# Performance work log

Measured on AMD Instinct MI355X. Metric: run time of the kernel, lower is better.

Reference implementation:

```python
import jax, jax.numpy as jnp
import numpy as np

N_NODES = 50000
N_EDGES = 800000
IN_CH = 512
HID = 256


def setup_inputs() -> dict:
    key = jax.random.key(0)
    ks = jax.random.split(key, 8)
    x = jax.random.normal(ks[0], (N_NODES, IN_CH), dtype=jnp.float32)
    edge_index = jax.random.randint(ks[1], (2, N_EDGES), 0, N_NODES, dtype=jnp.int64)
    # Glorot-ish init for weights
    W0 = jax.random.normal(ks[2], (IN_CH, HID), dtype=jnp.float32) / np.sqrt(IN_CH)
    W1 = jax.random.normal(ks[3], (HID, HID), dtype=jnp.float32) / np.sqrt(HID)
    W2 = jax.random.normal(ks[4], (HID, HID), dtype=jnp.float32) / np.sqrt(HID)
    Wout = jax.random.normal(ks[5], (HID, 1), dtype=jnp.float32) / np.sqrt(HID)
    return {
        "x": x, "edge_index": edge_index,
        "W0": W0, "b0": jnp.zeros((HID,), jnp.float32),
        "W1": W1, "b1": jnp.zeros((HID,), jnp.float32),
        "W2": W2, "b2": jnp.zeros((HID,), jnp.float32),
        "Wout": Wout, "bout": jnp.zeros((1,), jnp.float32),
    }


def _gcn_norm(edge_index, num_nodes):
    # Add self-loops, compute symmetric normalization D^-1/2 (A+I) D^-1/2
    loops = jnp.arange(num_nodes, dtype=edge_index.dtype)
    src = jnp.concatenate([edge_index[0], loops])
    dst = jnp.concatenate([edge_index[1], loops])
    ones = jnp.ones(src.shape[0], dtype=jnp.float32)
    deg = jax.ops.segment_sum(ones, dst, num_segments=num_nodes)
    dinv = jnp.where(deg > 0, jax.lax.rsqrt(deg), 0.0)
    norm = dinv[src] * dinv[dst]  # [E + N]
    return src, dst, norm


def _gcn_conv(x, src, dst, norm, W, b, num_nodes):
    h = x @ W                              # [N, out] dense GEMM first (PyG order)
    msg = h[src] * norm[:, None]           # gather + scale
    agg = jax.ops.segment_sum(msg, dst, num_segments=num_nodes)  # scatter-add
    return agg + b


def reference(x, edge_index, W0, b0, W1, b1, W2, b2, Wout, bout):
    n = x.shape[0]
    src, dst, norm = _gcn_norm(edge_index, n)
    h = jax.nn.relu(_gcn_conv(x, src, dst, norm, W0, b0, n))
    h = jax.nn.relu(_gcn_conv(h, src, dst, norm, W1, b1, n))
    h = jax.nn.relu(_gcn_conv(h, src, dst, norm, W2, b2, n))
    out = h @ Wout + bout                  # [N, 1] readout
    return out[:, 0]                       # squeeze(-1) -> [N]
```

## Files before the change

kernel.cpp:

```cpp
#include <hip/hip_runtime.h>

#define HID 256
#define IN_CH 512
#define NPAD 50176

typedef __attribute__((ext_vector_type(8))) short s16x8;
typedef __attribute__((ext_vector_type(4))) float f32x4;
typedef __attribute__((ext_vector_type(4))) _Float16 f16x4;

#define GLBP(p) ((const __attribute__((address_space(1))) void*)(p))
#define LDSP(p) ((__attribute__((address_space(3))) void*)(p))


__global__ __launch_bounds__(256) void k_count(const int* __restrict__ dst,
                                               int* __restrict__ cnt, int E) {
    int e = blockIdx.x * 256 + threadIdx.x;
    if (e < E) atomicAdd(&cnt[dst[e]], 1);
}

__global__ __launch_bounds__(256) void k_scan_bsum(const int* __restrict__ cnt,
                                                   int* __restrict__ bsum, int n) {
    __shared__ int sdata[256];
    int t = threadIdx.x;
    int base = blockIdx.x * 1024 + t * 4;
    int s = 0;
#pragma unroll
    for (int j = 0; j < 4; ++j) if (base + j < n) s += cnt[base + j];
    sdata[t] = s;
    __syncthreads();
    for (int off = 128; off > 0; off >>= 1) {
        if (t < off) sdata[t] += sdata[t + off];
        __syncthreads();
    }
    if (t == 0) bsum[blockIdx.x] = sdata[0];
}

__global__ __launch_bounds__(64) void k_scan_boff(const int* __restrict__ bsum,
                                                  int* __restrict__ boff, int nb) {
    int lane = threadIdx.x;
    int own = (lane < nb) ? bsum[lane] : 0;
    int v = own;
    for (int off = 1; off < 64; off <<= 1) {
        int u = __shfl_up(v, off, 64);
        if (lane >= off) v += u;
    }
    if (lane < nb) boff[lane] = v - own;
}

__global__ __launch_bounds__(256) void k_scan_write(const int* __restrict__ cnt,
                                                    const int* __restrict__ boff,
                                                    int* __restrict__ rowptr,
                                                    float* __restrict__ dinv, int n) {
    __shared__ int sdata[256];
    int t = threadIdx.x;
    int base = blockIdx.x * 1024 + t * 4;
    int c0 = (base + 0 < n) ? cnt[base + 0] : 0;
    int c1 = (base + 1 < n) ? cnt[base + 1] : 0;
    int c2 = (base + 2 < n) ? cnt[base + 2] : 0;
    int c3 = (base + 3 < n) ? cnt[base + 3] : 0;
    int tsum = c0 + c1 + c2 + c3;
    sdata[t] = tsum;
    __syncthreads();
    for (int off = 1; off < 256; off <<= 1) {
        int v = (t >= off) ? sdata[t - off] : 0;
        __syncthreads();
        if (t >= off) sdata[t] += v;
        __syncthreads();
    }
    int excl = sdata[t] - tsum;
    int p = boff[blockIdx.x] + excl;
    if (base + 0 < n) { rowptr[base + 1] = p + c0;                dinv[base + 0] = rsqrtf((float)(c0 + 1)); }
    if (base + 1 < n) { rowptr[base + 2] = p + c0 + c1;           dinv[base + 1] = rsqrtf((float)(c1 + 1)); }
    if (base + 2 < n) { rowptr[base + 3] = p + c0 + c1 + c2;      dinv[base + 2] = rsqrtf((float)(c2 + 1)); }
    if (base + 3 < n) { rowptr[base + 4] = p + c0 + c1 + c2 + c3; dinv[base + 3] = rsqrtf((float)(c3 + 1)); }
    if (blockIdx.x == 0 && t == 0) rowptr[0] = 0;
}

__global__ __launch_bounds__(256) void k_fill(const int* __restrict__ src,
                                              const int* __restrict__ dst,
                                              const int* __restrict__ rowptr,
                                              int* __restrict__ cursor,
                                              const float* __restrict__ dinv,
                                              int2* __restrict__ erec, int E) {
    int e = blockIdx.x * 256 + threadIdx.x;
    if (e >= E) return;
    int d = dst[e];
    int s = src[e];
    int pos = rowptr[d] + atomicAdd(&cursor[d], 1);
    float w = dinv[s] * dinv[d];
    erec[pos] = make_int2(s, __float_as_int(w));
}


__device__ __forceinline__ void wsplit_one(const float* W, unsigned short* Bt, int idx) {
    int n = idx & 255;
    int k = idx >> 8;
    float w = W[(size_t)k * HID + n];
    unsigned int u = __float_as_uint(w);
    unsigned short hi = (unsigned short)(u >> 16);
    float hif = __uint_as_float(u & 0xffff0000u);
    float lo = w - hif;
    unsigned short lob = (unsigned short)(__float_as_uint(lo) >> 16);
    unsigned short* p = Bt + (size_t)(k >> 5) * (HID * 104) + n * 104 + 3 * (k & 31);
    p[0] = hi; p[1] = hi; p[2] = lob;
}

__global__ __launch_bounds__(256) void k_wsplit3(const float* __restrict__ W0,
                                                 const float* __restrict__ W1,
                                                 const float* __restrict__ W2,
                                                 unsigned short* __restrict__ Bt0,
                                                 unsigned short* __restrict__ Bt1,
                                                 unsigned short* __restrict__ Bt2) {
    int t = blockIdx.x * 256 + threadIdx.x;
    if (t < IN_CH * HID) wsplit_one(W0, Bt0, t);
    else if (t < IN_CH * HID + HID * HID) wsplit_one(W1, Bt1, t - IN_CH * HID);
    else wsplit_one(W2, Bt2, t - IN_CH * HID - HID * HID);
}


template<bool RELU>
__global__ __launch_bounds__(512, 6) void k_gemm_mfma(const float* __restrict__ A,
                                                      const unsigned short* __restrict__ Bt,
                                                      _Float16* __restrict__ C16,
                                                      int M, int Korig) {
    __shared__ unsigned short Als[128 * 104];
    __shared__ unsigned short Bls[128 * 104];

    const int m0 = blockIdx.x * 128;
    const int n0 = blockIdx.y * 128;
    const int tid = threadIdx.x;
    const int wave = tid >> 6;
    const int lane = tid & 63;
    const int wm = wave >> 2;
    const int wn = wave & 3;

    f32x4 acc[4][2] = {};

    const int nsteps = Korig >> 5;
    const int arow = tid >> 2;
    const int aseg = (tid & 3) * 8;

    for (int ks = 0; ks < nsteps; ++ks) {
        {
            int gm = m0 + arow;
            float4 v0 = make_float4(0, 0, 0, 0), v1 = v0;
            if (gm < M) {
                const float* ap = A + (size_t)gm * Korig + ks * 32 + aseg;
                v0 = *(const float4*)ap;
                v1 = *(const float4*)(ap + 4);
            }
            float av[8] = {v0.x, v0.y, v0.z, v0.w, v1.x, v1.y, v1.z, v1.w};
            unsigned short hi[8], lo[8];
#pragma unroll
            for (int j = 0; j < 8; ++j) {
                float a = av[j];
                if (RELU) a = fmaxf(a, 0.f);
                unsigned int u = __float_as_uint(a);
                hi[j] = (unsigned short)(u >> 16);
                float hif = __uint_as_float(u & 0xffff0000u);
                float l = a - hif;
                lo[j] = (unsigned short)(__float_as_uint(l) >> 16);
            }
            s16x8 w0 = {(short)hi[0], (short)lo[0], (short)hi[0], (short)hi[1],
                        (short)lo[1], (short)hi[1], (short)hi[2], (short)lo[2]};
            s16x8 w1 = {(short)hi[2], (short)hi[3], (short)lo[3], (short)hi[3],
                        (short)hi[4], (short)lo[4], (short)hi[4], (short)hi[5]};
            s16x8 w2 = {(short)lo[5], (short)hi[5], (short)hi[6], (short)lo[6],
                        (short)hi[6], (short)hi[7], (short)lo[7], (short)hi[7]};
            s16x8* dp = (s16x8*)&Als[arow * 104 + (tid & 3) * 24];
            dp[0] = w0; dp[1] = w1; dp[2] = w2;
        }
        {
            const char* src = (const char*)(Bt + (size_t)ks * (HID * 104) + (size_t)n0 * 104);
            for (int g = wave; g < 26; g += 8) {
                int byteoff = (g * 64 + lane) * 16;
                __builtin_amdgcn_global_load_lds(GLBP(src + byteoff),
                                                 LDSP((char*)Bls + byteoff), 16, 0, 0);
            }
        }
        __syncthreads();

#pragma unroll
        for (int kk = 0; kk < 3; ++kk) {
            int gsh = (kk * 4 + (lane >> 4)) * 8;
            s16x8 af[4], bf[2];
#pragma unroll
            for (int mf = 0; mf < 4; ++mf) {
                int row = wm * 64 + mf * 16 + (lane & 15);
                af[mf] = *(const s16x8*)&Als[row * 104 + gsh];
            }
#pragma unroll
            for (int nf = 0; nf < 2; ++nf) {
                int col = wn * 32 + nf * 16 + (lane & 15);
                bf[nf] = *(const s16x8*)&Bls[col * 104 + gsh];
            }
#pragma unroll
            for (int mf = 0; mf < 4; ++mf)
#pragma unroll
                for (int nf = 0; nf < 2; ++nf)
                    acc[mf][nf] = __builtin_amdgcn_mfma_f32_16x16x32_bf16(af[mf], bf[nf],
                                                                          acc[mf][nf], 0, 0, 0);
        }
        __syncthreads();
    }

#pragma unroll
    for (int mf = 0; mf < 4; ++mf) {
        int row0 = m0 + wm * 64 + mf * 16 + (lane >> 4) * 4;
#pragma unroll
        for (int r = 0; r < 4; ++r) {
            int gr = row0 + r;
            if (gr < M) {
#pragma unroll
                for (int nf = 0; nf < 2; ++nf) {
                    int col = n0 + wn * 32 + nf * 16 + (lane & 15);
                    C16[(size_t)gr * HID + col] = (_Float16)acc[mf][nf][r];
                }
            }
        }
    }
}


template<bool READOUT>
__global__ __launch_bounds__(256) void k_aggregate(const _Float16* __restrict__ h,
                                                   const float* __restrict__ dinv,
                                                   const int* __restrict__ rowptr,
                                                   const int2* __restrict__ erec,
                                                   const float* __restrict__ bias,
                                                   float* __restrict__ agg,
                                                   const float* __restrict__ wout,
                                                   const float* __restrict__ bout,
                                                   float* __restrict__ out,
                                                   int n) {
    int node = blockIdx.x * 4 + (threadIdx.x >> 6);
    if (node >= n) return;
    int lane = threadIdx.x & 63;

    float dd = dinv[node];
    float4 acc;
    {
        float w = dd * dd;
        f16x4 v = *(const f16x4*)(h + (size_t)node * HID + lane * 4);
        float4 b = *(const float4*)(bias + lane * 4);
        acc = make_float4(b.x + (float)v[0] * w, b.y + (float)v[1] * w,
                          b.z + (float)v[2] * w, b.w + (float)v[3] * w);
    }

    int e = rowptr[node];
    int e_end = rowptr[node + 1];
    for (; e + 1 < e_end; e += 2) {
        int2 r0 = erec[e];
        int2 r1 = erec[e + 1];
        float w0 = __int_as_float(r0.y);
        float w1 = __int_as_float(r1.y);
        f16x4 v0 = *(const f16x4*)(h + (size_t)r0.x * HID + lane * 4);
        f16x4 v1 = *(const f16x4*)(h + (size_t)r1.x * HID + lane * 4);
        acc.x += (float)v0[0] * w0 + (float)v1[0] * w1;
        acc.y += (float)v0[1] * w0 + (float)v1[1] * w1;
        acc.z += (float)v0[2] * w0 + (float)v1[2] * w1;
        acc.w += (float)v0[3] * w0 + (float)v1[3] * w1;
    }
    if (e < e_end) {
        int2 r0 = erec[e];
        float w0 = __int_as_float(r0.y);
        f16x4 v0 = *(const f16x4*)(h + (size_t)r0.x * HID + lane * 4);
        acc.x += (float)v0[0] * w0; acc.y += (float)v0[1] * w0;
        acc.z += (float)v0[2] * w0; acc.w += (float)v0[3] * w0;
    }

    if (!READOUT) {
        *(float4*)(agg + (size_t)node * HID + lane * 4) = acc;
    } else {
        float4 w = *(const float4*)(wout + lane * 4);
        acc.x = fmaxf(acc.x, 0.f); acc.y = fmaxf(acc.y, 0.f);
        acc.z = fmaxf(acc.z, 0.f); acc.w = fmaxf(acc.w, 0.f);
        float s = acc.x * w.x + acc.y * w.y + acc.z * w.z + acc.w * w.w;
#pragma unroll
        for (int off = 32; off > 0; off >>= 1) s += __shfl_down(s, off, 64);
        if (lane == 0) out[node] = s + bout[0];
    }
}


extern "C" void kernel_launch(void* const* d_in, const int* in_sizes, int n_in,
                              void* d_out, int out_size, void* d_ws, size_t ws_size,
                              hipStream_t stream) {
    const float* x    = (const float*)d_in[0];
    const int*   ei   = (const int*)d_in[1];
    const float* W0   = (const float*)d_in[2];
    const float* b0   = (const float*)d_in[3];
    const float* W1   = (const float*)d_in[4];
    const float* b1   = (const float*)d_in[5];
    const float* W2   = (const float*)d_in[6];
    const float* b2   = (const float*)d_in[7];
    const float* Wout = (const float*)d_in[8];
    const float* bout = (const float*)d_in[9];
    float* out = (float*)d_out;

    const int n = in_sizes[0] / IN_CH;
    const int E = in_sizes[1] / 2;
    const int* src = ei;
    const int* dst = ei + E;

    float* dinv   = (float*)d_ws;
    int*   rowptr = (int*)(dinv + NPAD);
    int*   cursor = rowptr + NPAD;
    int2*  erec   = (int2*)(cursor + NPAD);
    int*   bsum   = (int*)(erec + 800000);
    int*   boff   = bsum + 64;
    unsigned short* Bt0 = (unsigned short*)(boff + 64);
    unsigned short* Bt1 = Bt0 + 16 * HID * 104;
    unsigned short* Bt2 = Bt1 + 8 * HID * 104;
    _Float16* h16 = (_Float16*)(Bt2 + 8 * HID * 104);
    float* agg32  = (float*)(h16 + (size_t)n * HID);

    const int nb_e = (E + 255) / 256;
    const int nb_scan = (n + 1023) / 1024;

    hipMemsetAsync(cursor, 0, (size_t)n * 4, stream);
    k_count<<<nb_e, 256, 0, stream>>>(dst, cursor, E);
    k_scan_bsum<<<nb_scan, 256, 0, stream>>>(cursor, bsum, n);
    k_scan_boff<<<1, 64, 0, stream>>>(bsum, boff, nb_scan);
    k_scan_write<<<nb_scan, 256, 0, stream>>>(cursor, boff, rowptr, dinv, n);
    hipMemsetAsync(cursor, 0, (size_t)n * 4, stream);
    k_fill<<<nb_e, 256, 0, stream>>>(src, dst, rowptr, cursor, dinv, erec, E);

    k_wsplit3<<<(IN_CH * HID + 2 * HID * HID) / 256, 256, 0, stream>>>(W0, W1, W2, Bt0, Bt1, Bt2);

    dim3 gg((n + 127) / 128, 2);
    const int agg_blocks = (n + 3) / 4;

    k_gemm_mfma<false><<<gg, 512, 0, stream>>>(x, Bt0, h16, n, IN_CH);
    k_aggregate<false><<<agg_blocks, 256, 0, stream>>>(h16, dinv, rowptr, erec, b0,
                                                       agg32, nullptr, nullptr, nullptr, n);
    k_gemm_mfma<true><<<gg, 512, 0, stream>>>(agg32, Bt1, h16, n, HID);
    k_aggregate<false><<<agg_blocks, 256, 0, stream>>>(h16, dinv, rowptr, erec, b1,
                                                       agg32, nullptr, nullptr, nullptr, n);
    k_gemm_mfma<true><<<gg, 512, 0, stream>>>(agg32, Bt2, h16, n, HID);
    k_aggregate<true><<<agg_blocks, 256, 0, stream>>>(h16, dinv, rowptr, erec, b2,
                                                      nullptr, Wout, bout, out, n);
}
```

Measured before the change: 584.7 us.

## Widen GEMM tile to full 256 columns and use granule-major LDS layout

The MFMA GEMM now computes all 256 output columns per block instead of splitting N across two blocks, so each A tile is loaded and split into bf16 hi/lo once rather than twice. Each wave holds a 4x4 accumulator grid. A and B are stored in LDS in a granule-major layout (16-byte granules indexed by k-group then row), and the weight pre-split kernel writes B in the matching layout. This removes the padded 104-stride layout and halves redundant A reads and conversions, at the cost of more registers per wave, more LDS per block and half as many blocks.

```diff
diff --git a/kernel.cpp b/kernel.cpp
--- a/kernel.cpp
+++ b/kernel.cpp
@@ -3,6 +3,9 @@
 #define HID 256
 #define IN_CH 512
 #define NPAD 50176
+
+#define NGRAN 12
+#define BTSTEP (NGRAN * 256 * 8)
 
 typedef __attribute__((ext_vector_type(8))) short s16x8;
 typedef __attribute__((ext_vector_type(4))) float f32x4;
@@ -101,8 +104,12 @@
     float hif = __uint_as_float(u & 0xffff0000u);
     float lo = w - hif;
     unsigned short lob = (unsigned short)(__float_as_uint(lo) >> 16);
-    unsigned short* p = Bt + (size_t)(k >> 5) * (HID * 104) + n * 104 + 3 * (k & 31);
-    p[0] = hi; p[1] = hi; p[2] = lob;
+    unsigned short* base = Bt + (size_t)(k >> 5) * BTSTEP;
+    int kz = k & 31;
+    int e0 = 3 * kz, e1 = e0 + 1, e2 = e0 + 2;
+    base[((e0 >> 3) * 256 + n) * 8 + (e0 & 7)] = hi;
+    base[((e1 >> 3) * 256 + n) * 8 + (e1 & 7)] = hi;
+    base[((e2 >> 3) * 256 + n) * 8 + (e2 & 7)] = lob;
 }
 
 __global__ __launch_bounds__(256) void k_wsplit3(const float* __restrict__ W0,
@@ -119,33 +126,32 @@
 
 
 template<bool RELU>
-__global__ __launch_bounds__(512, 6) void k_gemm_mfma(const float* __restrict__ A,
-                                                      const unsigned short* __restrict__ Bt,
-                                                      _Float16* __restrict__ C16,
-                                                      int M, int Korig) {
-    __shared__ unsigned short Als[128 * 104];
-    __shared__ unsigned short Bls[128 * 104];
+__global__ __launch_bounds__(512) void k_gemm_mfma(const float* __restrict__ A,
+                                                   const unsigned short* __restrict__ Bt,
+                                                   _Float16* __restrict__ C16,
+                                                   int M, int Korig) {
+    __shared__ s16x8 AlsG[NGRAN * 128];
+    __shared__ s16x8 BlsG[NGRAN * 256];
 
     const int m0 = blockIdx.x * 128;
-    const int n0 = blockIdx.y * 128;
     const int tid = threadIdx.x;
     const int wave = tid >> 6;
     const int lane = tid & 63;
     const int wm = wave >> 2;
     const int wn = wave & 3;
 
-    f32x4 acc[4][2] = {};
+    f32x4 acc[4][4] = {};
 
     const int nsteps = Korig >> 5;
     const int arow = tid >> 2;
-    const int aseg = (tid & 3) * 8;
+    const int at   = tid & 3;
 
     for (int ks = 0; ks < nsteps; ++ks) {
         {
             int gm = m0 + arow;
             float4 v0 = make_float4(0, 0, 0, 0), v1 = v0;
             if (gm < M) {
-                const float* ap = A + (size_t)gm * Korig + ks * 32 + aseg;
+                const float* ap = A + (size_t)gm * Korig + ks * 32 + at * 8;
                 v0 = *(const float4*)ap;
                 v1 = *(const float4*)(ap + 4);
             }
@@ -167,37 +173,38 @@
                         (short)hi[4], (short)lo[4], (short)hi[4], (short)hi[5]};
             s16x8 w2 = {(short)lo[5], (short)hi[5], (short)hi[6], (short)lo[6],
                         (short)hi[6], (short)hi[7], (short)lo[7], (short)hi[7]};
-            s16x8* dp = (s16x8*)&Als[arow * 104 + (tid & 3) * 24];
-            dp[0] = w0; dp[1] = w1; dp[2] = w2;
+            AlsG[(3 * at + 0) * 128 + arow] = w0;
+            AlsG[(3 * at + 1) * 128 + arow] = w1;
+            AlsG[(3 * at + 2) * 128 + arow] = w2;
         }
         {
-            const char* src = (const char*)(Bt + (size_t)ks * (HID * 104) + (size_t)n0 * 104);
-            for (int g = wave; g < 26; g += 8) {
+            const char* src = (const char*)(Bt + (size_t)ks * BTSTEP);
+            for (int g = wave; g < 48; g += 8) {
                 int byteoff = (g * 64 + lane) * 16;
                 __builtin_amdgcn_global_load_lds(GLBP(src + byteoff),
-                                                 LDSP((char*)Bls + byteoff), 16, 0, 0);
+                                                 LDSP((char*)BlsG + byteoff), 16, 0, 0);
             }
         }
         __syncthreads();
 
 #pragma unroll
         for (int kk = 0; kk < 3; ++kk) {
-            int gsh = (kk * 4 + (lane >> 4)) * 8;
-            s16x8 af[4], bf[2];
+            int g = kk * 4 + (lane >> 4);
+            s16x8 af[4], bf[4];
 #pragma unroll
             for (int mf = 0; mf < 4; ++mf) {
                 int row = wm * 64 + mf * 16 + (lane & 15);
-                af[mf] = *(const s16x8*)&Als[row * 104 + gsh];
-            }
-#pragma unroll
-            for (int nf = 0; nf < 2; ++nf) {
-                int col = wn * 32 + nf * 16 + (lane & 15);
-                bf[nf] = *(const s16x8*)&Bls[col * 104 + gsh];
+                af[mf] = AlsG[g * 128 + row];
+            }
+#pragma unroll
+            for (int nf = 0; nf < 4; ++nf) {
+                int col = wn * 64 + nf * 16 + (lane & 15);
+                bf[nf] = BlsG[g * 256 + col];
             }
 #pragma unroll
             for (int mf = 0; mf < 4; ++mf)
 #pragma unroll
-                for (int nf = 0; nf < 2; ++nf)
+                for (int nf = 0; nf < 4; ++nf)
                     acc[mf][nf] = __builtin_amdgcn_mfma_f32_16x16x32_bf16(af[mf], bf[nf],
                                                                           acc[mf][nf], 0, 0, 0);
         }
@@ -212,8 +219,8 @@
             int gr = row0 + r;
             if (gr < M) {
 #pragma unroll
-                for (int nf = 0; nf < 2; ++nf) {
-                    int col = n0 + wn * 32 + nf * 16 + (lane & 15);
+                for (int nf = 0; nf < 4; ++nf) {
+                    int col = wn * 64 + nf * 16 + (lane & 15);
                     C16[(size_t)gr * HID + col] = (_Float16)acc[mf][nf][r];
                 }
             }
@@ -310,9 +317,9 @@
     int*   bsum   = (int*)(erec + 800000);
     int*   boff   = bsum + 64;
     unsigned short* Bt0 = (unsigned short*)(boff + 64);
-    unsigned short* Bt1 = Bt0 + 16 * HID * 104;
-    unsigned short* Bt2 = Bt1 + 8 * HID * 104;
-    _Float16* h16 = (_Float16*)(Bt2 + 8 * HID * 104);
+    unsigned short* Bt1 = Bt0 + 16 * BTSTEP;
+    unsigned short* Bt2 = Bt1 + 8 * BTSTEP;
+    _Float16* h16 = (_Float16*)(Bt2 + 8 * BTSTEP);
     float* agg32  = (float*)(h16 + (size_t)n * HID);
 
     const int nb_e = (E + 255) / 256;
@@ -328,16 +335,16 @@
 
     k_wsplit3<<<(IN_CH * HID + 2 * HID * HID) / 256, 256, 0, stream>>>(W0, W1, W2, Bt0, Bt1, Bt2);
 
-    dim3 gg((n + 127) / 128, 2);
+    const int gemm_blocks = (n + 127) / 128;
     const int agg_blocks = (n + 3) / 4;
 
-    k_gemm_mfma<false><<<gg, 512, 0, stream>>>(x, Bt0, h16, n, IN_CH);
+    k_gemm_mfma<false><<<gemm_blocks, 512, 0, stream>>>(x, Bt0, h16, n, IN_CH);
     k_aggregate<false><<<agg_blocks, 256, 0, stream>>>(h16, dinv, rowptr, erec, b0,
                                                        agg32, nullptr, nullptr, nullptr, n);
-    k_gemm_mfma<true><<<gg, 512, 0, stream>>>(agg32, Bt1, h16, n, HID);
+    k_gemm_mfma<true><<<gemm_blocks, 512, 0, stream>>>(agg32, Bt1, h16, n, HID);
     k_aggregate<false><<<agg_blocks, 256, 0, stream>>>(h16, dinv, rowptr, erec, b1,
                                                        agg32, nullptr, nullptr, nullptr, n);
-    k_gemm_mfma<true><<<gg, 512, 0, stream>>>(agg32, Bt2, h16, n, HID);
+    k_gemm_mfma<true><<<gemm_blocks, 512, 0, stream>>>(agg32, Bt2, h16, n, HID);
     k_aggregate<true><<<agg_blocks, 256, 0, stream>>>(h16, dinv, rowptr, erec, b2,
                                                       nullptr, Wout, bout, out, n);
 }
```

New measurement: 545.9 us. 6.6% less time.
